# Kernel tuning notes

Measured on AMD Instinct MI355X. Metric: run time of the kernel, lower is better.

Reference implementation:

```python
import jax, jax.numpy as jnp
import numpy as np

B, S, D = 8, 2048, 768


def setup_inputs() -> dict:
    key = jax.random.key(0)
    ks = jax.random.split(key, 16)
    def lin(kw, kb, din, dout):
        # torch nn.Linear default init: U(-1/sqrt(din), 1/sqrt(din))
        bound = 1.0 / np.sqrt(din)
        W = jax.random.uniform(kw, (din, dout), minval=-bound, maxval=bound, dtype=jnp.float32)
        b = jax.random.uniform(kb, (dout,), minval=-bound, maxval=bound, dtype=jnp.float32)
        return W, b
    Wq1, bq1 = lin(ks[0], ks[1], D, D)
    Wk1, bk1 = lin(ks[2], ks[3], D, D)
    Wv1, bv1 = lin(ks[4], ks[5], D, D)
    Wq2, bq2 = lin(ks[6], ks[7], D, D)
    Wk2, bk2 = lin(ks[8], ks[9], D, D)
    Wv2, bv2 = lin(ks[10], ks[11], D, D)
    Wf, bf = lin(ks[12], ks[13], 2 * D, D)
    self_x = jax.random.normal(ks[14], (B, S, D), dtype=jnp.float32)
    conv_x = jax.random.normal(ks[15], (B, S, D), dtype=jnp.float32)
    return {
        "self_x": self_x, "conv_x": conv_x,
        "Wq1": Wq1, "bq1": bq1, "Wk1": Wk1, "bk1": bk1, "Wv1": Wv1, "bv1": bv1,
        "Wq2": Wq2, "bq2": bq2, "Wk2": Wk2, "bk2": bk2, "Wv2": Wv2, "bv2": bv2,
        "Wf": Wf, "bf": bf,
    }


def reference(self_x, conv_x, Wq1, bq1, Wk1, bk1, Wv1, bv1,
              Wq2, bq2, Wk2, bk2, Wv2, bv2, Wf, bf):
    scale = jnp.asarray(Wk1.shape[-1] ** 0.5, dtype=self_x.dtype)

    # direction 1: queries from self_x, keys/values from conv_x
    Q1 = self_x @ Wq1 + bq1            # [B,S,D]
    K1 = conv_x @ Wk1 + bk1
    V1 = conv_x @ Wv1 + bv1
    attn1 = jnp.einsum('bqd,bkd->bqk', Q1, K1) / scale
    # NOTE: softmax over dim=1 (the QUERY axis), as in the original module
    w1 = jax.nn.softmax(attn1, axis=1)
    attn_out1 = jnp.einsum('bqk,bkd->bqd', w1, V1)

    # direction 2: queries from conv_x, keys/values from self_x
    Q2 = conv_x @ Wq2 + bq2
    K2 = self_x @ Wk2 + bk2
    V2 = self_x @ Wv2 + bv2
    attn2 = jnp.einsum('bqd,bkd->bqk', Q2, K2) / scale
    w2 = jax.nn.softmax(attn2, axis=1)
    attn_out2 = jnp.einsum('bqk,bkd->bqd', w2, V2)

    a1 = jax.nn.sigmoid(jnp.tanh(attn_out1))
    a2 = jax.nn.sigmoid(jnp.tanh(attn_out2))
    out1 = a2 * self_x + (1.0 - a2) * conv_x
    out2 = a1 * conv_x + (1.0 - a1) * self_x
    fused = jnp.concatenate([out1, out2], axis=-1)  # [B,S,2D]
    return fused @ Wf + bf
```

## Files before the change

kernel.cpp:

```cpp
#include <hip/hip_runtime.h>
#include <hip/hip_bf16.h>

#define BM 128
#define BN 128
#define BK 64

typedef short short8 __attribute__((ext_vector_type(8)));
typedef float f32x4 __attribute__((ext_vector_type(4)));

using bf = __hip_bfloat16;

static const int NOSPLIT = 1 << 30;

__device__ __forceinline__ void gld16(const void* g, void* l)
{
    __builtin_amdgcn_global_load_lds(
        (__attribute__((address_space(1))) void*)g,
        (__attribute__((address_space(3))) void*)l, 16, 0, 0);
}

__device__ __forceinline__ int lofs(int row, int kg8)
{
    return row * 64 + ((kg8 ^ (row & 7)) << 3);
}

__global__ __launch_bounds__(256)
void cast_bf16(const float* __restrict__ src, bf* __restrict__ dst, int n)
{
    int i = (blockIdx.x * 256 + threadIdx.x) * 4;
    if (i >= n) return;
    float4 v = *(const float4*)(src + i);
    bf o[4] = { __float2bfloat16(v.x), __float2bfloat16(v.y),
                __float2bfloat16(v.z), __float2bfloat16(v.w) };
    *(uint2*)(dst + i) = *(const uint2*)o;
}

__global__ __launch_bounds__(256)
void transpose_cast_w(const float* __restrict__ W, bf* __restrict__ Wt,
                      int Kd, int Nd)
{
    __shared__ float tile[32][33];
    int k0 = blockIdx.y * 32, n0 = blockIdx.x * 32;
    int t = threadIdx.x;
    int r = t >> 3, c = (t & 7) * 4;
    float4 v = *(const float4*)(W + (size_t)(k0 + r) * Nd + n0 + c);
    tile[r][c] = v.x; tile[r][c+1] = v.y; tile[r][c+2] = v.z; tile[r][c+3] = v.w;
    __syncthreads();
    bf o[4] = { __float2bfloat16(tile[c][r]),   __float2bfloat16(tile[c+1][r]),
                __float2bfloat16(tile[c+2][r]), __float2bfloat16(tile[c+3][r]) };
    *(uint2*)(Wt + (size_t)(n0 + r) * Kd + k0 + c) = *(const uint2*)o;
}

template <typename CT, bool TC>
__global__ __launch_bounds__(256)
void gemm_nt(const bf* __restrict__ A, const bf* __restrict__ A2, int splitA, int lda,
             const bf* __restrict__ Bt, int ldb,
             const float* __restrict__ bias, CT* __restrict__ C, int ldc,
             int K, long long strA, long long strB, long long strC)
{
    __shared__ __align__(16) ushort sA[BM * 64];
    __shared__ __align__(16) ushort sB[BN * 64];

    const int z = blockIdx.z;
    A  += (long long)z * strA;
    A2 += (long long)z * strA;
    Bt += (long long)z * strB;
    C  += (long long)z * strC;

    const int t = threadIdx.x;
    const int m0 = blockIdx.x * BM;
    const int n0 = blockIdx.y * BN;
    const int wave = t >> 6, lane = t & 63;
    const int wm = wave >> 1, wn = wave & 1;
    const int lcol = lane & 15, quad = lane >> 4;
    const int rl = lane >> 3, cslot = lane & 7;

    f32x4 acc[4][4] = {};

    for (int kt = 0; kt < K; kt += BK) {
        const bf* Asrc = (kt < splitA) ? A : A2;
        const int ktt = (kt < splitA) ? kt : kt - splitA;
        #pragma unroll
        for (int it = 0; it < 4; ++it) {
            int br  = it * 32 + wave * 8;
            int row = br + rl;
            int kg  = cslot ^ rl;
            gld16(Asrc + (size_t)(m0 + row) * lda + ktt + kg * 8, &sA[br * 64]);
            gld16(Bt   + (size_t)(n0 + row) * ldb + kt  + kg * 8, &sB[br * 64]);
        }
        __syncthreads();

        #pragma unroll
        for (int h = 0; h < 2; ++h) {
            short8 af[4], bfr[4];
            #pragma unroll
            for (int i = 0; i < 4; ++i)
                af[i] = *(const short8*)&sA[lofs(wm * 64 + i * 16 + lcol, h * 4 + quad)];
            #pragma unroll
            for (int j = 0; j < 4; ++j)
                bfr[j] = *(const short8*)&sB[lofs(wn * 64 + j * 16 + lcol, h * 4 + quad)];
            #pragma unroll
            for (int i = 0; i < 4; ++i)
                #pragma unroll
                for (int j = 0; j < 4; ++j)
                    acc[i][j] = __builtin_amdgcn_mfma_f32_16x16x32_bf16(af[i], bfr[j], acc[i][j], 0, 0, 0);
        }
        __syncthreads();
    }

    #pragma unroll
    for (int j = 0; j < 4; ++j) {
        int col = n0 + wn * 64 + j * 16 + lcol;
        float bv = bias ? bias[col] : 0.0f;
        #pragma unroll
        for (int i = 0; i < 4; ++i) {
            int row = m0 + wm * 64 + i * 16 + quad * 4;
            if (!TC) {
                #pragma unroll
                for (int r4 = 0; r4 < 4; ++r4)
                    C[(size_t)(row + r4) * ldc + col] = (CT)(acc[i][j][r4] + bv);
            } else {
                bf o[4];
                #pragma unroll
                for (int r4 = 0; r4 < 4; ++r4)
                    o[r4] = __float2bfloat16(acc[i][j][r4] + bv);
                *(uint2*)((bf*)C + (size_t)col * ldc + row) = *(const uint2*)o;
            }
        }
    }
}

__global__ __launch_bounds__(256)
void scores_exp(const bf* __restrict__ Q, const bf* __restrict__ Km,
                bf* __restrict__ E, float* __restrict__ colsum,
                int Dd, float rscale)
{
    const int S = 2048;
    __shared__ __align__(16) ushort sA[BM * 64];
    __shared__ __align__(16) ushort sB[BN * 64];

    const int z = blockIdx.z;
    Q  += (size_t)z * S * Dd;
    Km += (size_t)z * S * Dd;
    E  += (size_t)z * S * S;
    colsum += (size_t)z * S;

    const int t = threadIdx.x;
    const int m0 = blockIdx.x * BM;
    const int n0 = blockIdx.y * BN;
    const int wave = t >> 6, lane = t & 63;
    const int wm = wave >> 1, wn = wave & 1;
    const int lcol = lane & 15, quad = lane >> 4;
    const int rl = lane >> 3, cslot = lane & 7;

    f32x4 acc[4][4] = {};

    for (int kt = 0; kt < Dd; kt += BK) {
        #pragma unroll
        for (int it = 0; it < 4; ++it) {
            int br  = it * 32 + wave * 8;
            int row = br + rl;
            int kg  = cslot ^ rl;
            gld16(Q  + (size_t)(m0 + row) * Dd + kt + kg * 8, &sA[br * 64]);
            gld16(Km + (size_t)(n0 + row) * Dd + kt + kg * 8, &sB[br * 64]);
        }
        __syncthreads();

        #pragma unroll
        for (int h = 0; h < 2; ++h) {
            short8 af[4], bfr[4];
            #pragma unroll
            for (int i = 0; i < 4; ++i)
                af[i] = *(const short8*)&sA[lofs(wm * 64 + i * 16 + lcol, h * 4 + quad)];
            #pragma unroll
            for (int j = 0; j < 4; ++j)
                bfr[j] = *(const short8*)&sB[lofs(wn * 64 + j * 16 + lcol, h * 4 + quad)];
            #pragma unroll
            for (int a = 0; a < 4; ++a)
                #pragma unroll
                for (int b = 0; b < 4; ++b)
                    acc[a][b] = __builtin_amdgcn_mfma_f32_16x16x32_bf16(bfr[a], af[b], acc[a][b], 0, 0, 0);
        }
        __syncthreads();
    }

    #pragma unroll
    for (int a = 0; a < 4; ++a) {
        const int kk = n0 + wn * 64 + a * 16 + quad * 4;
        f32x4 csum = {0.f, 0.f, 0.f, 0.f};
        #pragma unroll
        for (int b = 0; b < 4; ++b) {
            const int q = m0 + wm * 64 + b * 16 + lcol;
            bf o[4];
            #pragma unroll
            for (int r = 0; r < 4; ++r) {
                float e = __expf(acc[a][b][r] * rscale);
                o[r] = __float2bfloat16(e);
                csum[r] += e;
            }
            *(uint2*)(E + (size_t)q * S + kk) = *(const uint2*)o;
        }
        #pragma unroll
        for (int msk = 1; msk < 16; msk <<= 1) {
            csum[0] += __shfl_xor(csum[0], msk);
            csum[1] += __shfl_xor(csum[1], msk);
            csum[2] += __shfl_xor(csum[2], msk);
            csum[3] += __shfl_xor(csum[3], msk);
        }
        if (lcol == 0) {
            atomicAdd(&colsum[kk + 0], csum[0]);
            atomicAdd(&colsum[kk + 1], csum[1]);
            atomicAdd(&colsum[kk + 2], csum[2]);
            atomicAdd(&colsum[kk + 3], csum[3]);
        }
    }
}

__global__ __launch_bounds__(256)
void scale_vt(bf* __restrict__ Vt, const float* __restrict__ cs, int ldv)
{
    int col = (blockIdx.x * 256 + threadIdx.x) * 4;
    bf* p = Vt + (size_t)blockIdx.y * ldv + col;
    bf v[4]; *(uint2*)v = *(const uint2*)p;
    float4 c4 = *(const float4*)(cs + col);
    v[0] = __float2bfloat16(__bfloat162float(v[0]) / c4.x);
    v[1] = __float2bfloat16(__bfloat162float(v[1]) / c4.y);
    v[2] = __float2bfloat16(__bfloat162float(v[2]) / c4.z);
    v[3] = __float2bfloat16(__bfloat162float(v[3]) / c4.w);
    *(uint2*)p = *(const uint2*)v;
}

__global__ __launch_bounds__(256)
void gate_fuse(const bf* __restrict__ O1, const bf* __restrict__ O2,
               const float* __restrict__ SX, const float* __restrict__ CX,
               bf* __restrict__ F1, bf* __restrict__ F2, int n)
{
    int i = (blockIdx.x * 256 + threadIdx.x) * 4;
    if (i >= n) return;
    bf o1[4], o2[4], f1[4], f2[4];
    *(uint2*)o1 = *(const uint2*)(O1 + i);
    *(uint2*)o2 = *(const uint2*)(O2 + i);
    float4 sx = *(const float4*)(SX + i);
    float4 cx = *(const float4*)(CX + i);
    #pragma unroll
    for (int e = 0; e < 4; ++e) {
        float s = (&sx.x)[e], c = (&cx.x)[e];
        float a1 = 1.0f / (1.0f + __expf(-tanhf(__bfloat162float(o1[e]))));
        float a2 = 1.0f / (1.0f + __expf(-tanhf(__bfloat162float(o2[e]))));
        f1[e] = __float2bfloat16(a2 * s + (1.0f - a2) * c);
        f2[e] = __float2bfloat16(a1 * c + (1.0f - a1) * s);
    }
    *(uint2*)(F1 + i) = *(const uint2*)f1;
    *(uint2*)(F2 + i) = *(const uint2*)f2;
}

extern "C" void kernel_launch(void* const* d_in, const int* in_sizes, int n_in,
                              void* d_out, int out_size, void* d_ws, size_t ws_size,
                              hipStream_t stream)
{
    const int B = 8, S = 2048, D = 768;
    const int M = B * S;

    const float* SX = (const float*)d_in[0];
    const float* CX = (const float*)d_in[1];
    const float* Wsrc[7] = { (const float*)d_in[2],  (const float*)d_in[4],
                             (const float*)d_in[6],  (const float*)d_in[8],
                             (const float*)d_in[10], (const float*)d_in[12],
                             (const float*)d_in[14] };
    const float* bias[7] = { (const float*)d_in[3],  (const float*)d_in[5],
                             (const float*)d_in[7],  (const float*)d_in[9],
                             (const float*)d_in[11], (const float*)d_in[13],
                             (const float*)d_in[15] };
    float* out = (float*)d_out;

    char* w = (char*)d_ws;
    const size_t MD  = (size_t)M * D * sizeof(bf);
    const size_t WSZ = (size_t)D * D * sizeof(bf);
    const size_t SSB = (size_t)S * S * sizeof(bf);
    bf* Xs = (bf*)(w);
    bf* Xc = (bf*)(w + MD);
    bf* Wt[7];
    for (int i = 0; i < 7; ++i) Wt[i] = (bf*)(w + 2 * MD + i * WSZ);
    char* base2 = w + 2 * MD + 8 * WSZ;
    bf* Q  = (bf*)(base2);
    bf* Kb = (bf*)(base2 + MD);
    bf* Vt = (bf*)(base2 + 2 * MD);
    bf* O1 = (bf*)(base2 + 3 * MD);
    float* cs = (float*)(base2 + 4 * MD);
    char* Eb0 = base2 + 4 * MD + (size_t)2 * B * S * sizeof(float);
    bf* E = (bf*)Eb0;
    int cb;
    {
        size_t fixed = (size_t)(Eb0 - w);
        size_t avail = ws_size > fixed ? ws_size - fixed : SSB;
        long long c = (long long)(avail / SSB);
        cb = c < 1 ? 1 : (c > 8 ? 8 : (int)c);
    }
    bf* O2 = Xs;
    bf* F1 = Kb;
    bf* F2 = Vt;

    (void)hipMemsetAsync(cs, 0, (size_t)2 * B * S * sizeof(float), stream);

    dim3 blk(256);
    {
        int n = M * D;
        cast_bf16<<<dim3(n / 1024), blk, 0, stream>>>(SX, Xs, n);
        cast_bf16<<<dim3(n / 1024), blk, 0, stream>>>(CX, Xc, n);
        for (int i = 0; i < 6; ++i)
            transpose_cast_w<<<dim3(D / 32, D / 32), blk, 0, stream>>>(Wsrc[i], Wt[i], D, D);
        transpose_cast_w<<<dim3(D / 32, 2 * D / 32), blk, 0, stream>>>(Wsrc[6], Wt[6], 2 * D, D);
    }

    dim3 gProj(M / BM, D / BN);
    const float rscale = 1.0f / sqrtf((float)D);
    const size_t SD = (size_t)S * D;
    const long long SS = (long long)S * S;

    for (int dir = 0; dir < 2; ++dir) {
        const bf* Xq = dir == 0 ? Xs : Xc;
        const bf* Xk = dir == 0 ? Xc : Xs;
        bf* Wq = Wt[dir * 3 + 0];
        bf* Wk = Wt[dir * 3 + 1];
        bf* Wv = Wt[dir * 3 + 2];
        const float* bq = bias[dir * 3 + 0];
        const float* bk = bias[dir * 3 + 1];
        const float* bv = bias[dir * 3 + 2];
        bf* O = dir == 0 ? O1 : O2;
        float* csd = cs + (size_t)dir * B * S;

        gemm_nt<bf, false><<<gProj, blk, 0, stream>>>(Xq, Xq, NOSPLIT, D, Wq, D, bq, Q,  D, D, 0, 0, 0);
        gemm_nt<bf, false><<<gProj, blk, 0, stream>>>(Xk, Xk, NOSPLIT, D, Wk, D, bk, Kb, D, D, 0, 0, 0);
        gemm_nt<bf, true ><<<gProj, blk, 0, stream>>>(Xk, Xk, NOSPLIT, D, Wv, D, bv, Vt, M, D, 0, 0, 0);

        for (int c0 = 0; c0 < B; c0 += cb) {
            int cbc = (B - c0 < cb) ? (B - c0) : cb;
            scores_exp<<<dim3(S / BM, S / BN, cbc), blk, 0, stream>>>(
                Q + c0 * SD, Kb + c0 * SD, E, csd + (size_t)c0 * S, D, rscale);
            scale_vt<<<dim3(cbc * S / 1024, D), blk, 0, stream>>>(
                Vt + (size_t)c0 * S, csd + (size_t)c0 * S, M);
            gemm_nt<bf, false><<<dim3(S / BM, D / BN, cbc), blk, 0, stream>>>(
                E, E, NOSPLIT, S, Vt + (size_t)c0 * S, M, nullptr,
                O + c0 * SD, D, S, SS, S, (long long)SD);
        }
    }

    gate_fuse<<<dim3(M * D / 1024), blk, 0, stream>>>(O1, O2, SX, CX, F1, F2, M * D);
    gemm_nt<float, false><<<gProj, blk, 0, stream>>>(F1, F2, D, D, Wt[6], 2 * D,
                                                     bias[6], out, D, 2 * D, 0, 0, 0);
}
```

Baseline: 747.1 us.

## Double-buffer LDS tiles in GEMM and score kernels to overlap loads with MFMA

Both the generic NT GEMM and the fused scores/exp kernel now keep two LDS buffers per operand. The next K-tile is issued with global_load_lds into the alternate buffer before the MFMA work on the current tile, and the loop keeps one barrier per iteration instead of two. The goal is to hide global-to-LDS latency behind matrix-core compute. In exchange, LDS per block doubles to 64 KB, which can lower the number of resident blocks per CU.

```diff
diff --git a/kernel.cpp b/kernel.cpp
--- a/kernel.cpp
+++ b/kernel.cpp
@@ -58,8 +58,8 @@
              const float* __restrict__ bias, CT* __restrict__ C, int ldc,
              int K, long long strA, long long strB, long long strC)
 {
-    __shared__ __align__(16) ushort sA[BM * 64];
-    __shared__ __align__(16) ushort sB[BN * 64];
+    __shared__ __align__(16) ushort sA[2][BM * 64];
+    __shared__ __align__(16) ushort sB[2][BN * 64];
 
     const int z = blockIdx.z;
     A  += (long long)z * strA;
@@ -75,9 +75,7 @@
     const int lcol = lane & 15, quad = lane >> 4;
     const int rl = lane >> 3, cslot = lane & 7;
 
-    f32x4 acc[4][4] = {};
-
-    for (int kt = 0; kt < K; kt += BK) {
+    auto stage = [&](int kt, int c) {
         const bf* Asrc = (kt < splitA) ? A : A2;
         const int ktt = (kt < splitA) ? kt : kt - splitA;
         #pragma unroll
@@ -85,20 +83,28 @@
             int br  = it * 32 + wave * 8;
             int row = br + rl;
             int kg  = cslot ^ rl;
-            gld16(Asrc + (size_t)(m0 + row) * lda + ktt + kg * 8, &sA[br * 64]);
-            gld16(Bt   + (size_t)(n0 + row) * ldb + kt  + kg * 8, &sB[br * 64]);
-        }
-        __syncthreads();
+            gld16(Asrc + (size_t)(m0 + row) * lda + ktt + kg * 8, &sA[c][br * 64]);
+            gld16(Bt   + (size_t)(n0 + row) * ldb + kt  + kg * 8, &sB[c][br * 64]);
+        }
+    };
+
+    f32x4 acc[4][4] = {};
+
+    stage(0, 0);
+    __syncthreads();
+    int cur = 0;
+    for (int kt = 0; kt < K; kt += BK) {
+        if (kt + BK < K) stage(kt + BK, cur ^ 1);
 
         #pragma unroll
         for (int h = 0; h < 2; ++h) {
             short8 af[4], bfr[4];
             #pragma unroll
             for (int i = 0; i < 4; ++i)
-                af[i] = *(const short8*)&sA[lofs(wm * 64 + i * 16 + lcol, h * 4 + quad)];
+                af[i] = *(const short8*)&sA[cur][lofs(wm * 64 + i * 16 + lcol, h * 4 + quad)];
             #pragma unroll
             for (int j = 0; j < 4; ++j)
-                bfr[j] = *(const short8*)&sB[lofs(wn * 64 + j * 16 + lcol, h * 4 + quad)];
+                bfr[j] = *(const short8*)&sB[cur][lofs(wn * 64 + j * 16 + lcol, h * 4 + quad)];
             #pragma unroll
             for (int i = 0; i < 4; ++i)
                 #pragma unroll
@@ -106,6 +112,7 @@
                     acc[i][j] = __builtin_amdgcn_mfma_f32_16x16x32_bf16(af[i], bfr[j], acc[i][j], 0, 0, 0);
         }
         __syncthreads();
+        cur ^= 1;
     }
 
     #pragma unroll
@@ -136,8 +143,8 @@
                 int Dd, float rscale)
 {
     const int S = 2048;
-    __shared__ __align__(16) ushort sA[BM * 64];
-    __shared__ __align__(16) ushort sB[BN * 64];
+    __shared__ __align__(16) ushort sA[2][BM * 64];
+    __shared__ __align__(16) ushort sB[2][BN * 64];
 
     const int z = blockIdx.z;
     Q  += (size_t)z * S * Dd;
@@ -153,28 +160,34 @@
     const int lcol = lane & 15, quad = lane >> 4;
     const int rl = lane >> 3, cslot = lane & 7;
 
-    f32x4 acc[4][4] = {};
-
-    for (int kt = 0; kt < Dd; kt += BK) {
+    auto stage = [&](int kt, int c) {
         #pragma unroll
         for (int it = 0; it < 4; ++it) {
             int br  = it * 32 + wave * 8;
             int row = br + rl;
             int kg  = cslot ^ rl;
-            gld16(Q  + (size_t)(m0 + row) * Dd + kt + kg * 8, &sA[br * 64]);
-            gld16(Km + (size_t)(n0 + row) * Dd + kt + kg * 8, &sB[br * 64]);
-        }
-        __syncthreads();
+            gld16(Q  + (size_t)(m0 + row) * Dd + kt + kg * 8, &sA[c][br * 64]);
+            gld16(Km + (size_t)(n0 + row) * Dd + kt + kg * 8, &sB[c][br * 64]);
+        }
+    };
+
+    f32x4 acc[4][4] = {};
+
+    stage(0, 0);
+    __syncthreads();
+    int cur = 0;
+    for (int kt = 0; kt < Dd; kt += BK) {
+        if (kt + BK < Dd) stage(kt + BK, cur ^ 1);
 
         #pragma unroll
         for (int h = 0; h < 2; ++h) {
             short8 af[4], bfr[4];
             #pragma unroll
             for (int i = 0; i < 4; ++i)
-                af[i] = *(const short8*)&sA[lofs(wm * 64 + i * 16 + lcol, h * 4 + quad)];
+                af[i] = *(const short8*)&sA[cur][lofs(wm * 64 + i * 16 + lcol, h * 4 + quad)];
             #pragma unroll
             for (int j = 0; j < 4; ++j)
-                bfr[j] = *(const short8*)&sB[lofs(wn * 64 + j * 16 + lcol, h * 4 + quad)];
+                bfr[j] = *(const short8*)&sB[cur][lofs(wn * 64 + j * 16 + lcol, h * 4 + quad)];
             #pragma unroll
             for (int a = 0; a < 4; ++a)
                 #pragma unroll
@@ -182,6 +195,7 @@
                     acc[a][b] = __builtin_amdgcn_mfma_f32_16x16x32_bf16(bfr[a], af[b], acc[a][b], 0, 0, 0);
         }
         __syncthreads();
+        cur ^= 1;
     }
 
     #pragma unroll
```

After: 842.8 us. 1.13x slower.
